# Optimization experiments

Measured on AMD Instinct MI355X. Metric: run time of the kernel, lower is better.

Reference implementation:

```python
import jax, jax.numpy as jnp
import numpy as np

EPS = 1e-8


def setup_inputs() -> dict:
    key = jax.random.key(0)
    k1, k2, k3, k4 = jax.random.split(key, 4)
    B, Cin, Cout, K, S, H, W = 8, 512, 512, 3, 512, 64, 64
    return {
        "x": jax.random.normal(k1, (B, Cin, H, W), dtype=jnp.float32),
        "style": jax.random.normal(k2, (B, S), dtype=jnp.float32),
        "weight": jax.random.normal(k3, (1, Cout, Cin, K, K), dtype=jnp.float32),
        "mod_w": jax.random.normal(k4, (Cin, S), dtype=jnp.float32),
        "mod_b": jnp.ones((Cin,), dtype=jnp.float32),
    }


def reference(x, style, weight, mod_w, mod_b):
    B, Cin, H, W = x.shape
    Cout, K = weight.shape[1], weight.shape[-1]
    style_dim = mod_w.shape[1]
    conv_scale = 1.0 / np.sqrt(Cin * K * K)  # 1/sqrt(fan_in)
    mod_scale = 1.0 / np.sqrt(style_dim)     # EqualLinear scale (lr_mul=1)

    # EqualLinear modulation: (B, Cin)
    s = style @ (mod_w * mod_scale).T + mod_b

    # per-sample modulated weights: (B, Cout, Cin, K, K)
    w = conv_scale * weight * s[:, None, :, None, None]
    demod = jax.lax.rsqrt(jnp.sum(w * w, axis=(2, 3, 4)) + EPS)  # (B, Cout)
    w = w * demod[:, :, None, None, None]

    # grouped conv with groups = batch
    w = w.reshape(B * Cout, Cin, K, K)
    xg = x.reshape(1, B * Cin, H, W)
    pad = (K - 1) // 2
    out = jax.lax.conv_general_dilated(
        xg, w,
        window_strides=(1, 1),
        padding=[(pad, pad), (pad, pad)],
        dimension_numbers=("NCHW", "OIHW", "NCHW"),
        feature_group_count=B,
    )
    return out.reshape(B, Cout, out.shape[2], out.shape[3])
```

## Files before the change

### kernel.cpp

```cpp
#include <hip/hip_runtime.h>
#include <hip/hip_bf16.h>
#include <cstdint>
#include <cstddef>

typedef __bf16 bf16x8 __attribute__((ext_vector_type(8)));
typedef float f32x4 __attribute__((ext_vector_type(4)));
typedef unsigned int uintx4 __attribute__((ext_vector_type(4)));

#define CONV_SCALE 0.014731391274719738f
#define MOD_SCALE  0.044194173824159216f

__device__ __forceinline__ unsigned short f2bf(float v) {
  unsigned int u = __float_as_uint(v);
  return (unsigned short)((u + 0x7FFFu + ((u >> 16) & 1u)) >> 16);
}

__device__ __forceinline__ void gload16(const void* g, void* l) {
  __builtin_amdgcn_global_load_lds(
      (const __attribute__((address_space(1))) unsigned int*)g,
      (__attribute__((address_space(3))) unsigned int*)l, 16, 0, 0);
}

__global__ void k_prep1(const float* __restrict__ style,
                        const float* __restrict__ mod_w,
                        const float* __restrict__ mod_b,
                        const float* __restrict__ weight,
                        float* __restrict__ s,
                        unsigned short* __restrict__ wT,
                        float* __restrict__ wsq) {
  __shared__ float lds[4608];
  int t = threadIdx.x;
  if (blockIdx.x < 512) {
    int co = blockIdx.x;
    const float* w = weight + (size_t)co * 4608;
    #pragma unroll
    for (int i = 0; i < 18; ++i) lds[t + i * 256] = w[t + i * 256];
    __syncthreads();
    for (int i = t; i < 576; i += 256) {
      int tap = i / 64, c8 = (i & 63) * 8;
      union { uintx4 v; unsigned short us[8]; } pk;
      #pragma unroll
      for (int j = 0; j < 8; ++j) pk.us[j] = f2bf(lds[(c8 + j) * 9 + tap]);
      *(uintx4*)(wT + ((size_t)tap * 512 + co) * 512 + c8) = pk.v;
    }
    for (int ci = t; ci < 512; ci += 256) {
      float a = 0.f;
      #pragma unroll
      for (int tap = 0; tap < 9; ++tap) { float v = lds[ci * 9 + tap]; a += v * v; }
      wsq[co * 512 + ci] = a * (CONV_SCALE * CONV_SCALE);
    }
  } else {
    int blk = blockIdx.x - 512;
    int b = blk >> 2, ch = blk & 3;
    int ci = ch * 128 + (t >> 1), half = t & 1;
    const float* st = style + b * 512 + half * 256;
    const float* mw = mod_w + (size_t)ci * 512 + half * 256;
    float acc = 0.f;
    #pragma unroll 8
    for (int k = 0; k < 256; k += 4) {
      f32x4 a = *(const f32x4*)(st + k);
      f32x4 m = *(const f32x4*)(mw + k);
      acc += a[0] * m[0] + a[1] * m[1] + a[2] * m[2] + a[3] * m[3];
    }
    acc += __shfl_xor(acc, 1);
    if (half == 0) s[b * 512 + ci] = acc * MOD_SCALE + mod_b[ci];
  }
}

__global__ void k_prep2(const float* __restrict__ x,
                        const float* __restrict__ s,
                        const float* __restrict__ wsq,
                        unsigned short* __restrict__ xT,
                        float* __restrict__ demod) {
  __shared__ float lds[128][68];
  int t = threadIdx.x;
  int id = blockIdx.x;
  if (id < 2048) {
    int cc = id & 3, h = (id >> 2) & 63, b = id >> 8;
    int w4 = (t & 15) * 4, rr = t >> 4;
    #pragma unroll
    for (int i = 0; i < 8; ++i) {
      int ci = i * 16 + rr;
      *(f32x4*)&lds[ci][w4] =
          *(const f32x4*)&x[(((size_t)(b * 512 + cc * 128 + ci)) * 64 + h) * 64 + w4];
    }
    __syncthreads();
    int pos = t >> 2, c4 = t & 3;
    #pragma unroll
    for (int q = 0; q < 4; ++q) {
      int cb = q * 32 + c4 * 8;
      union { uintx4 v; unsigned short us[8]; } pk;
      #pragma unroll
      for (int j = 0; j < 8; ++j) {
        int ci = cb + j;
        pk.us[j] = f2bf(lds[ci][pos] * s[b * 512 + cc * 128 + ci]);
      }
      *(uintx4*)(xT + (((size_t)(b * 64 + h)) * 64 + pos) * 512 + cc * 128 + cb) = pk.v;
    }
  } else {
    int blk = id - 2048;
    int b = blk >> 1;
    int co = (blk & 1) * 256 + t;
    const float* wq = wsq + (size_t)co * 512;
    const float* sb = s + b * 512;
    float acc = 0.f;
    #pragma unroll 4
    for (int ci = 0; ci < 512; ci += 4) {
      f32x4 q = *(const f32x4*)(wq + ci);
      f32x4 v = *(const f32x4*)(sb + ci);
      acc += q[0] * v[0] * v[0] + q[1] * v[1] * v[1] + q[2] * v[2] * v[2] + q[3] * v[3] * v[3];
    }
    demod[b * 512 + co] = rsqrtf(acc + 1e-8f);
  }
}

__global__ __launch_bounds__(512, 2) void k_conv(
    const unsigned short* __restrict__ xT,
    const unsigned short* __restrict__ wT,
    const float* __restrict__ demod,
    float* __restrict__ out) {
  extern __shared__ __align__(16) char lds_raw[];
  char* xb0   = lds_raw;
  char* xb1   = lds_raw + 42240;
  char* wring = lds_raw + 84480;
  char* trash = lds_raw + 117248;

  const int id  = blockIdx.x;
  const int g_ord = (id & 7) * 32 + (id >> 3);
  const int co_t  = g_ord >> 6;
  const int slice = g_ord & 63;
  const int b   = slice >> 3;
  const int h_t = slice & 7;

  const int t = threadIdx.x;
  const int lane = t & 63, wv = t >> 6;
  const int h0  = h_t * 8;
  const int co0 = co_t * 128;
  const int l15 = lane & 15, kg = lane >> 4;
  const int wrow = wv & 3;
  const int wco  = wv >> 2;

  {
    uintx4 z = {0u, 0u, 0u, 0u};
    for (int i = t; i < 5280; i += 512) ((uintx4*)lds_raw)[i] = z;
  }
  __syncthreads();

  auto xstage = [&](int j, int ccs, char* xbuf) {
    int r = j >> 2, k = j & 3;
    int hh = h0 - 1 + r;
    int hc = ((unsigned)hh < 64u) ? hh : 0;
    int p = r * 66 + 1 + k * 16 + (lane >> 2);
    const void* src = xT + (((size_t)(b * 64 + hc)) * 64 + k * 16 + (lane >> 2)) * 512
                      + ccs * 32 + (((lane & 3) ^ ((p >> 1) & 3)) << 3);
    void* dst = ((unsigned)hh < 64u) ? (void*)(xbuf + (r * 66 + 1 + k * 16) * 64)
                                     : (void*)trash;
    gload16(src, dst);
  };
  auto wstage = [&](int g) {
    int gc = (g <= 143) ? g : 143;
    int s = g & 3;
    int cc2 = gc / 9, tap2 = gc - cc2 * 9;
    int row0 = wv * 16;
    int row = row0 + (lane >> 2);
    const void* src = wT + ((size_t)tap2 * 512 + co0 + row) * 512
                      + cc2 * 32 + (((lane & 3) ^ ((row >> 1) & 3)) << 3);
    void* dst = (g <= 143) ? (void*)(wring + s * 8192 + row0 * 64) : (void*)trash;
    gload16(src, dst);
  };

  f32x4 acc[4][2][4] = {};

  #pragma unroll
  for (int i = 0; i < 5; ++i) xstage(wv * 5 + i, 0, xb0);
  wstage(0);
  wstage(1);
  __syncthreads();

  #pragma unroll 1
  for (int cc = 0; cc < 16; ++cc) {
    const char* xcur = (cc & 1) ? xb1 : xb0;
    char* xnxt = (cc & 1) ? xb0 : xb1;
    const int ccs = (cc + 1) & 15;
    #pragma unroll
    for (int tap = 0; tap < 9; ++tap) {
      if (tap == 0 || tap == 1 || tap == 7 || tap == 8)
        asm volatile("s_waitcnt vmcnt(1)" ::: "memory");
      else
        asm volatile("s_waitcnt vmcnt(2)" ::: "memory");

      const int g = cc * 9 + tap;
      const int s = g & 3;
      const int dh = tap / 3, dw = tap % 3;

      bf16x8 af[4], bfr[2][4];
      #pragma unroll
      for (int m = 0; m < 4; ++m) {
        int row = wco * 64 + m * 16 + l15;
        af[m] = *(const bf16x8*)(wring + s * 8192 + row * 64 + ((kg ^ ((row >> 1) & 3)) << 4));
      }
      #pragma unroll
      for (int r = 0; r < 2; ++r)
        #pragma unroll
        for (int n = 0; n < 4; ++n) {
          int p = (2 * wrow + r + dh) * 66 + n * 16 + l15 + dw;
          bfr[r][n] = *(const bf16x8*)(xcur + p * 64 + ((kg ^ ((p >> 1) & 3)) << 4));
        }

      wstage(g + 2);
      if (tap >= 1 && tap <= 5) xstage((tap - 1) * 8 + wv, ccs, xnxt);

      __builtin_amdgcn_s_barrier();

      __builtin_amdgcn_s_setprio(1);
      #pragma unroll
      for (int m = 0; m < 4; ++m)
        #pragma unroll
        for (int r = 0; r < 2; ++r)
          #pragma unroll
          for (int n = 0; n < 4; ++n)
            acc[m][r][n] = __builtin_amdgcn_mfma_f32_16x16x32_bf16(af[m], bfr[r][n], acc[m][r][n], 0, 0, 0);
      __builtin_amdgcn_s_setprio(0);
    }
  }

  #pragma unroll
  for (int m = 0; m < 4; ++m) {
    #pragma unroll
    for (int q = 0; q < 4; ++q) {
      int co = co0 + wco * 64 + m * 16 + kg * 4 + q;
      float scl = CONV_SCALE * demod[b * 512 + co];
      #pragma unroll
      for (int r = 0; r < 2; ++r) {
        int h_out = h0 + 2 * wrow + r;
        #pragma unroll
        for (int n = 0; n < 4; ++n) {
          out[(((size_t)(b * 512 + co)) * 64 + h_out) * 64 + n * 16 + l15] = acc[m][r][n][q] * scl;
        }
      }
    }
  }
}

extern "C" void kernel_launch(void* const* d_in, const int* in_sizes, int n_in,
                              void* d_out, int out_size, void* d_ws, size_t ws_size,
                              hipStream_t stream) {
  const float* x      = (const float*)d_in[0];
  const float* style  = (const float*)d_in[1];
  const float* weight = (const float*)d_in[2];
  const float* mod_w  = (const float*)d_in[3];
  const float* mod_b  = (const float*)d_in[4];
  float* out = (float*)d_out;

  char* ws = (char*)d_ws;
  unsigned short* xT = (unsigned short*)ws;
  unsigned short* wT = (unsigned short*)(ws + 33554432);
  float* s     = (float*)(ws + 38273024);
  float* wsq   = (float*)(ws + 38289408);
  float* demod = (float*)(ws + 39337984);

  static int lds_set = 0;
  if (!lds_set) {
    (void)hipFuncSetAttribute((const void*)k_conv,
                              hipFuncAttributeMaxDynamicSharedMemorySize, 118272);
    lds_set = 1;
  }

  hipLaunchKernelGGL(k_prep1, dim3(544),  dim3(256), 0, stream,
                     style, mod_w, mod_b, weight, s, wT, wsq);
  hipLaunchKernelGGL(k_prep2, dim3(2064), dim3(256), 0, stream, x, s, wsq, xT, demod);
  hipLaunchKernelGGL(k_conv,  dim3(256),  dim3(512), 118272, stream, xT, wT, demod, out);
}
```

Before: 163.8 us.

## Use a nine-slot weight ring and three barriers per channel chunk

The conv main loop now gives each of the nine taps its own LDS slot in the weight ring instead of a four-slot ring, and groups taps three at a time. That allows one barrier per three taps instead of one per tap, with weight and x loads for later phases issued in bulk and vmcnt waits adjusted to match. The cost being targeted is frequent workgroup synchronization and tight load/compute coupling in the MFMA loop. In exchange, LDS use rises to about 159KB, which rules out two blocks per CU, and each barrier covers a longer prefetch distance.

```diff
diff --git a/kernel.cpp b/kernel.cpp
--- a/kernel.cpp
+++ b/kernel.cpp
@@ -123,7 +123,7 @@
   char* xb0   = lds_raw;
   char* xb1   = lds_raw + 42240;
   char* wring = lds_raw + 84480;
-  char* trash = lds_raw + 117248;
+  char* trash = lds_raw + 158208;
 
   const int id  = blockIdx.x;
   const int g_ord = (id & 7) * 32 + (id >> 3);
@@ -157,24 +157,49 @@
                                      : (void*)trash;
     gload16(src, dst);
   };
-  auto wstage = [&](int g) {
-    int gc = (g <= 143) ? g : 143;
-    int s = g & 3;
-    int cc2 = gc / 9, tap2 = gc - cc2 * 9;
+  auto wstage = [&](int cc2, int tap2) {
+    bool valid = (cc2 < 16);
+    int cs = valid ? cc2 : 15;
     int row0 = wv * 16;
     int row = row0 + (lane >> 2);
     const void* src = wT + ((size_t)tap2 * 512 + co0 + row) * 512
-                      + cc2 * 32 + (((lane & 3) ^ ((row >> 1) & 3)) << 3);
-    void* dst = (g <= 143) ? (void*)(wring + s * 8192 + row0 * 64) : (void*)trash;
+                      + cs * 32 + (((lane & 3) ^ ((row >> 1) & 3)) << 3);
+    void* dst = valid ? (void*)(wring + tap2 * 8192 + row0 * 64) : (void*)trash;
     gload16(src, dst);
   };
 
   f32x4 acc[4][2][4] = {};
 
+  auto dotap = [&](const char* xcur, int T, int dh, int dw) {
+    bf16x8 af[4], bfr[2][4];
+    #pragma unroll
+    for (int m = 0; m < 4; ++m) {
+      int row = wco * 64 + m * 16 + l15;
+      af[m] = *(const bf16x8*)(wring + T * 8192 + row * 64 + ((kg ^ ((row >> 1) & 3)) << 4));
+    }
+    #pragma unroll
+    for (int r = 0; r < 2; ++r)
+      #pragma unroll
+      for (int n = 0; n < 4; ++n) {
+        int p = (2 * wrow + r + dh) * 66 + n * 16 + l15 + dw;
+        bfr[r][n] = *(const bf16x8*)(xcur + p * 64 + ((kg ^ ((p >> 1) & 3)) << 4));
+      }
+    __builtin_amdgcn_s_setprio(1);
+    #pragma unroll
+    for (int m = 0; m < 4; ++m)
+      #pragma unroll
+      for (int r = 0; r < 2; ++r)
+        #pragma unroll
+        for (int n = 0; n < 4; ++n)
+          acc[m][r][n] = __builtin_amdgcn_mfma_f32_16x16x32_bf16(af[m], bfr[r][n], acc[m][r][n], 0, 0, 0);
+    __builtin_amdgcn_s_setprio(0);
+  };
+
+  #pragma unroll
+  for (int i = 0; i < 6; ++i) wstage(0, i);
   #pragma unroll
   for (int i = 0; i < 5; ++i) xstage(wv * 5 + i, 0, xb0);
-  wstage(0);
-  wstage(1);
+  asm volatile("s_waitcnt vmcnt(0)" ::: "memory");
   __syncthreads();
 
   #pragma unroll 1
@@ -182,46 +207,24 @@
     const char* xcur = (cc & 1) ? xb1 : xb0;
     char* xnxt = (cc & 1) ? xb0 : xb1;
     const int ccs = (cc + 1) & 15;
-    #pragma unroll
-    for (int tap = 0; tap < 9; ++tap) {
-      if (tap == 0 || tap == 1 || tap == 7 || tap == 8)
-        asm volatile("s_waitcnt vmcnt(1)" ::: "memory");
-      else
-        asm volatile("s_waitcnt vmcnt(2)" ::: "memory");
-
-      const int g = cc * 9 + tap;
-      const int s = g & 3;
-      const int dh = tap / 3, dw = tap % 3;
-
-      bf16x8 af[4], bfr[2][4];
-      #pragma unroll
-      for (int m = 0; m < 4; ++m) {
-        int row = wco * 64 + m * 16 + l15;
-        af[m] = *(const bf16x8*)(wring + s * 8192 + row * 64 + ((kg ^ ((row >> 1) & 3)) << 4));
-      }
-      #pragma unroll
-      for (int r = 0; r < 2; ++r)
-        #pragma unroll
-        for (int n = 0; n < 4; ++n) {
-          int p = (2 * wrow + r + dh) * 66 + n * 16 + l15 + dw;
-          bfr[r][n] = *(const bf16x8*)(xcur + p * 64 + ((kg ^ ((p >> 1) & 3)) << 4));
-        }
-
-      wstage(g + 2);
-      if (tap >= 1 && tap <= 5) xstage((tap - 1) * 8 + wv, ccs, xnxt);
-
-      __builtin_amdgcn_s_barrier();
-
-      __builtin_amdgcn_s_setprio(1);
-      #pragma unroll
-      for (int m = 0; m < 4; ++m)
-        #pragma unroll
-        for (int r = 0; r < 2; ++r)
-          #pragma unroll
-          for (int n = 0; n < 4; ++n)
-            acc[m][r][n] = __builtin_amdgcn_mfma_f32_16x16x32_bf16(af[m], bfr[r][n], acc[m][r][n], 0, 0, 0);
-      __builtin_amdgcn_s_setprio(0);
-    }
+
+    asm volatile("s_waitcnt vmcnt(3)" ::: "memory");
+    __builtin_amdgcn_s_barrier();
+    xstage(wv, ccs, xnxt); xstage(wv + 8, ccs, xnxt);
+    wstage(cc, 6); wstage(cc, 7); wstage(cc, 8);
+    dotap(xcur, 0, 0, 0); dotap(xcur, 1, 0, 1); dotap(xcur, 2, 0, 2);
+
+    asm volatile("s_waitcnt vmcnt(5)" ::: "memory");
+    __builtin_amdgcn_s_barrier();
+    xstage(wv + 16, ccs, xnxt); xstage(wv + 24, ccs, xnxt);
+    wstage(cc + 1, 0); wstage(cc + 1, 1); wstage(cc + 1, 2);
+    dotap(xcur, 3, 1, 0); dotap(xcur, 4, 1, 1); dotap(xcur, 5, 1, 2);
+
+    asm volatile("s_waitcnt vmcnt(5)" ::: "memory");
+    __builtin_amdgcn_s_barrier();
+    xstage(wv + 32, ccs, xnxt);
+    wstage(cc + 1, 3); wstage(cc + 1, 4); wstage(cc + 1, 5);
+    dotap(xcur, 6, 2, 0); dotap(xcur, 7, 2, 1); dotap(xcur, 8, 2, 2);
   }
 
   #pragma unroll
@@ -262,12 +265,12 @@
   static int lds_set = 0;
   if (!lds_set) {
     (void)hipFuncSetAttribute((const void*)k_conv,
-                              hipFuncAttributeMaxDynamicSharedMemorySize, 118272);
+                              hipFuncAttributeMaxDynamicSharedMemorySize, 159232);
     lds_set = 1;
   }
 
   hipLaunchKernelGGL(k_prep1, dim3(544),  dim3(256), 0, stream,
                      style, mod_w, mod_b, weight, s, wT, wsq);
   hipLaunchKernelGGL(k_prep2, dim3(2064), dim3(256), 0, stream, x, s, wsq, xT, demod);
-  hipLaunchKernelGGL(k_conv,  dim3(256),  dim3(512), 118272, stream, xT, wT, demod, out);
-}
+  hipLaunchKernelGGL(k_conv,  dim3(256),  dim3(512), 159232, stream, xT, wT, demod, out);
+}
```

New measurement: 163.7 us. Within noise of the previous version (-0.1%).
